# Performance work log

Measured on AMD Instinct MI355X. Metric: run time of the kernel, lower is better.

The kernel has to match this reference:

```python
import jax, jax.numpy as jnp
import numpy as np

ALPHA = 0.2  # LeakyReLU negative slope


def setup_inputs() -> dict:
    key = jax.random.key(0)
    ks = jax.random.split(key, 6)
    B, N, F_IN, F_OUT = 4, 4096, 128, 128
    return {
        "input": jax.random.normal(ks[0], (B, N, F_IN), dtype=jnp.float32),
        "adj": jax.random.uniform(ks[1], (B, N, N), dtype=jnp.float32),
        "W": jax.random.normal(ks[2], (F_IN, F_OUT), dtype=jnp.float32) * (np.sqrt(2.0) / np.sqrt(F_IN)),
        "a1": jax.random.normal(ks[3], (F_OUT, 1), dtype=jnp.float32) * 0.1,
        "a2": jax.random.normal(ks[4], (F_OUT, 1), dtype=jnp.float32) * 0.1,
        "bias": jax.random.normal(ks[5], (N, F_OUT), dtype=jnp.float32) * 0.02,
    }


def reference(input, adj, W, a1, a2, bias):
    # h = X @ W : [B, N, F_out]
    h = jnp.einsum("bnf,fo->bno", input, W)
    # additive attention scores: e[b,i,j] = leakyrelu(f1[b,i] + f2[b,j])
    f1 = h @ a1            # [B, N, 1]
    f2 = h @ a2            # [B, N, 1]
    e = f1 + jnp.swapaxes(f2, 1, 2)        # [B, N, N]
    e = jnp.where(e >= 0, e, ALPHA * e)    # LeakyReLU
    # NOTE: original multiplies adj into scores (not -inf masking) and
    # softmaxes over dim=1 (the first node axis), faithfully reproduced.
    attention = jax.nn.softmax(adj * e, axis=1)  # [B, N, N]
    # dropout p=0 / eval mode -> identity
    h_prime = jnp.einsum("bij,bjo->bio", attention, h) + bias[None, :, :]
    # in_features == out_features -> plain residual
    return h_prime + input
```

## Files before the change

kernel.cpp:

```cpp
#include <hip/hip_runtime.h>
#include <hip/hip_bf16.h>

typedef short short8 __attribute__((ext_vector_type(8)));
typedef float f32x4 __attribute__((ext_vector_type(4)));
typedef unsigned short u16;
typedef u16 u16x4 __attribute__((ext_vector_type(4)));
typedef u16 u16x8 __attribute__((ext_vector_type(8)));

static constexpr float kAlpha = 0.2f;

static __device__ inline u16 f2bf(float f) {
  __hip_bfloat16 h = __float2bfloat16(f);
  return *reinterpret_cast<u16*>(&h);
}
static __device__ inline float bf2f(u16 v) {
  unsigned int u = ((unsigned int)v) << 16;
  return __uint_as_float(u);
}

__global__ __launch_bounds__(256) void k1_hW(const float* __restrict__ X,
                                             const float* __restrict__ W,
                                             const float* __restrict__ a1,
                                             const float* __restrict__ a2,
                                             u16* __restrict__ hbT,
                                             float* __restrict__ f1,
                                             float* __restrict__ f2) {
  int row0 = blockIdx.x * 8;
  int o = threadIdx.x & 127;
  int g = threadIdx.x >> 7;
  __shared__ float Xs[8][128];
#pragma unroll
  for (int s = 0; s < 4; ++s) {
    int idx = threadIdx.x + s * 256;
    Xs[idx >> 7][idx & 127] = X[(size_t)row0 * 128 + idx];
  }
  __syncthreads();
  float acc[4] = {0.f, 0.f, 0.f, 0.f};
  for (int k = 0; k < 128; ++k) {
    float w = W[k * 128 + o];
#pragma unroll
    for (int s = 0; s < 4; ++s) acc[s] += Xs[g + 2 * s][k] * w;
  }
  int b = row0 >> 12;
  int n0 = row0 & 4095;
#pragma unroll
  for (int s = 0; s < 4; ++s)
    hbT[((size_t)b * 128 + o) * 4096 + n0 + g + 2 * s] = f2bf(acc[s]);

  float a1o = a1[o], a2o = a2[o];
  __syncthreads();
#pragma unroll
  for (int s = 0; s < 4; ++s) Xs[g + 2 * s][o] = acc[s] * a1o;
  __syncthreads();
  int r = threadIdx.x >> 5, c = threadIdx.x & 31;
  float s1 = Xs[r][c] + Xs[r][c + 32] + Xs[r][c + 64] + Xs[r][c + 96];
  s1 += __shfl_xor(s1, 1);
  s1 += __shfl_xor(s1, 2);
  s1 += __shfl_xor(s1, 4);
  s1 += __shfl_xor(s1, 8);
  s1 += __shfl_xor(s1, 16);
  if (c == 0) f1[b * 4096 + n0 + r] = s1;
  __syncthreads();
#pragma unroll
  for (int s = 0; s < 4; ++s) Xs[g + 2 * s][o] = acc[s] * a2o;
  __syncthreads();
  float s2 = Xs[r][c] + Xs[r][c + 32] + Xs[r][c + 64] + Xs[r][c + 96];
  s2 += __shfl_xor(s2, 1);
  s2 += __shfl_xor(s2, 2);
  s2 += __shfl_xor(s2, 4);
  s2 += __shfl_xor(s2, 8);
  s2 += __shfl_xor(s2, 16);
  if (c == 0) f2[b * 4096 + n0 + r] = s2;
}

__global__ __launch_bounds__(256) void k2_dpart(const float* __restrict__ adj,
                                                const float* __restrict__ f1,
                                                const float* __restrict__ f2,
                                                float* __restrict__ dpart) {
  int bid = blockIdx.x;
  int ic = bid & 31;
  int jt = (bid >> 5) & 15;
  int b = bid >> 9;
  int t = threadIdx.x;
  int c = t & 63, r = t >> 6;
  int j = jt * 256 + c * 4;
  const size_t badj = (size_t)b * 4096 * 4096;
  f32x4 f2v = *reinterpret_cast<const f32x4*>(&f2[b * 4096 + j]);
  const float* f1p = f1 + b * 4096;
  int row0 = ic * 128 + r;
  f32x4 sum = (f32x4){0.f, 0.f, 0.f, 0.f};
#pragma unroll 8
  for (int s = 0; s < 32; ++s) {
    int row = row0 + 4 * s;
    f32x4 a = *reinterpret_cast<const f32x4*>(&adj[badj + (size_t)row * 4096 + j]);
    float f1r = f1p[row];
#pragma unroll
    for (int k = 0; k < 4; ++k) {
      float e = f1r + f2v[k];
      e = e >= 0.f ? e : kAlpha * e;
      sum[k] += __expf(a[k] * e);
    }
  }
  __shared__ f32x4 red[256];
  red[t] = sum;
  __syncthreads();
  if (t < 64) {
    f32x4 tt = red[t] + red[t + 64] + red[t + 128] + red[t + 192];
    *reinterpret_cast<f32x4*>(&dpart[(size_t)(b * 32 + ic) * 4096 + j]) = tt;
  }
}

__global__ __launch_bounds__(256) void k2b_scale(const float* __restrict__ dpart,
                                                 const u16* __restrict__ hbT,
                                                 u16* __restrict__ hs) {
  int bid = blockIdx.x;
  int og = bid & 7;
  int jb = (bid >> 3) & 15;
  int b = bid >> 7;
  int j = jb * 256 + threadIdx.x;
  float s = 0.f;
#pragma unroll
  for (int ic = 0; ic < 32; ++ic) s += dpart[(size_t)(b * 32 + ic) * 4096 + j];
  float rd = 1.0f / s;
  const u16* src = hbT + (size_t)b * 128 * 4096 + j;
  u16* dst = hs + (size_t)b * 128 * 4096 + j;
#pragma unroll 4
  for (int o = og * 16; o < og * 16 + 16; ++o) {
    dst[(size_t)o * 4096] = f2bf(bf2f(src[(size_t)o * 4096]) * rd);
  }
}

#define LROWW 72
#define BARRIER()                                      \
  {                                                    \
    asm volatile("s_waitcnt lgkmcnt(0)" ::: "memory"); \
    __builtin_amdgcn_s_barrier();                      \
  }
__global__ __launch_bounds__(512) void k3w(const float* __restrict__ adj,
                                           const u16* __restrict__ hs,
                                           const float* __restrict__ f1,
                                           const float* __restrict__ f2,
                                           float* __restrict__ parts) {
  int bid0 = blockIdx.x;
  int bid = ((bid0 & 7) << 5) | (bid0 >> 3);
  int b = bid >> 6;
  int it = (bid >> 2) & 15;
  int jq = bid & 3;
  int i0 = it * 256;
  int jbase = jq * 1024;
  int t = threadIdx.x;
  int lane = t & 63;
  int w = t >> 6;
  int rw = w & 3;
  int cw = w >> 2;

  __shared__ u16 As[2][256 * LROWW];
  __shared__ u16 Bs[2][128 * LROWW];

  const size_t badj = (size_t)b * 4096 * 4096;
  const u16* hb = hs + (size_t)b * 128 * 4096;
  const float* f2b = f2 + b * 4096;

  int r0 = t >> 4;
  int c0 = (t & 15) * 4;
  int bo = t >> 2;
  int bc0 = (t & 3) * 16;

  float f1v[8];
#pragma unroll
  for (int u = 0; u < 8; ++u) f1v[u] = f1[b * 4096 + i0 + r0 + 32 * u];

  int l15 = lane & 15;
  int l8 = (lane >> 4) * 8;

  f32x4 acc[4][4];
#pragma unroll
  for (int rg = 0; rg < 4; ++rg)
#pragma unroll
    for (int n = 0; n < 4; ++n) acc[rg][n] = (f32x4){0.f, 0.f, 0.f, 0.f};

  const float* ap0 = adj + badj + (size_t)(i0 + r0) * 4096 + c0;

  f32x4 raA0, raA1, raA2, raA3, raA4, raA5, raA6, raA7;
  f32x4 raB0, raB1, raB2, raB3, raB4, raB5, raB6, raB7;
  f32x4 rfA, rfB;
  u16x8 rbA0, rbA1, rbB0, rbB1;

#define PF(S, JO)                                                         \
  {                                                                       \
    int jj = jbase + ((JO) & 1023);    \
    const float* ap = ap0 + jj;                                           \
    ra##S##0 = *reinterpret_cast<const f32x4*>(ap);                       \
    ra##S##1 = *reinterpret_cast<const f32x4*>(ap + (size_t)1 * 131072);  \
    ra##S##2 = *reinterpret_cast<const f32x4*>(ap + (size_t)2 * 131072);  \
    ra##S##3 = *reinterpret_cast<const f32x4*>(ap + (size_t)3 * 131072);  \
    ra##S##4 = *reinterpret_cast<const f32x4*>(ap + (size_t)4 * 131072);  \
    ra##S##5 = *reinterpret_cast<const f32x4*>(ap + (size_t)5 * 131072);  \
    ra##S##6 = *reinterpret_cast<const f32x4*>(ap + (size_t)6 * 131072);  \
    ra##S##7 = *reinterpret_cast<const f32x4*>(ap + (size_t)7 * 131072);  \
    rf##S = *reinterpret_cast<const f32x4*>(f2b + jj + c0);               \
    const u16* bp = hb + (size_t)bo * 4096 + jj + bc0;                    \
    rb##S##0 = *reinterpret_cast<const u16x8*>(bp);                       \
    rb##S##1 = *reinterpret_cast<const u16x8*>(bp + 8);                   \
  }

#define STU(S, U, BUF)                                                    \
  {                                                                       \
    u16x4 pv;                                                             \
    _Pragma("unroll") for (int k = 0; k < 4; ++k) {                       \
      float e = f1v[U] + rf##S[k];                                        \
      e = e >= 0.f ? e : kAlpha * e;                                      \
      pv[k] = f2bf(__expf(ra##S##U[k] * e));                              \
    }                                                                     \
    *reinterpret_cast<u16x4*>(&As[BUF][(r0 + 32 * U) * LROWW + c0]) = pv; \
  }

#define STORE(S, BUF)                                                     \
  {                                                                       \
    STU(S, 0, BUF) STU(S, 1, BUF) STU(S, 2, BUF) STU(S, 3, BUF)           \
    STU(S, 4, BUF) STU(S, 5, BUF) STU(S, 6, BUF) STU(S, 7, BUF)           \
    *reinterpret_cast<u16x8*>(&Bs[BUF][bo * LROWW + bc0]) = rb##S##0;     \
    *reinterpret_cast<u16x8*>(&Bs[BUF][bo * LROWW + bc0 + 8]) = rb##S##1; \
  }

#define DOMFMA(BUF)                                                                \
  {                                                                                \
    _Pragma("unroll") for (int kk = 0; kk < 64; kk += 32) {                        \
      short8 af0 = *reinterpret_cast<const short8*>(                               \
          &As[BUF][(rw * 64 + 0 * 16 + l15) * LROWW + kk + l8]);                   \
      short8 af1 = *reinterpret_cast<const short8*>(                               \
          &As[BUF][(rw * 64 + 1 * 16 + l15) * LROWW + kk + l8]);                   \
      short8 af2 = *reinterpret_cast<const short8*>(                               \
          &As[BUF][(rw * 64 + 2 * 16 + l15) * LROWW + kk + l8]);                   \
      short8 af3 = *reinterpret_cast<const short8*>(                               \
          &As[BUF][(rw * 64 + 3 * 16 + l15) * LROWW + kk + l8]);                   \
      _Pragma("unroll") for (int n = 0; n < 4; ++n) {                              \
        short8 bf = *reinterpret_cast<const short8*>(                              \
            &Bs[BUF][(cw * 64 + n * 16 + l15) * LROWW + kk + l8]);                 \
        acc[0][n] = __builtin_amdgcn_mfma_f32_16x16x32_bf16(af0, bf, acc[0][n], 0, 0, 0); \
        acc[1][n] = __builtin_amdgcn_mfma_f32_16x16x32_bf16(af1, bf, acc[1][n], 0, 0, 0); \
        acc[2][n] = __builtin_amdgcn_mfma_f32_16x16x32_bf16(af2, bf, acc[2][n], 0, 0, 0); \
        acc[3][n] = __builtin_amdgcn_mfma_f32_16x16x32_bf16(af3, bf, acc[3][n], 0, 0, 0); \
      }                                                                            \
    }                                                                              \
  }

  PF(A, 0);
  PF(B, 64);

  for (int j0 = 0; j0 < 1024; j0 += 128) {
    STORE(A, 0);
    BARRIER();
    DOMFMA(0);
    PF(A, j0 + 128);
    STORE(B, 1);
    BARRIER();
    DOMFMA(1);
    PF(B, j0 + 192);
  }

  float* pq = parts + (size_t)(b * 4 + jq) * 4096 * 128;
#pragma unroll
  for (int rg = 0; rg < 4; ++rg) {
#pragma unroll
    for (int n = 0; n < 4; ++n) {
      int o = cw * 64 + n * 16 + l15;
#pragma unroll
      for (int q = 0; q < 4; ++q) {
        int i = i0 + rw * 64 + rg * 16 + (lane >> 4) * 4 + q;
        pq[(size_t)i * 128 + o] = acc[rg][n][q];
      }
    }
  }
}

__global__ __launch_bounds__(256) void k4r(const float* __restrict__ parts,
                                           const float* __restrict__ bias,
                                           const float* __restrict__ input,
                                           float* __restrict__ out) {
  size_t v = (size_t)blockIdx.x * 256 + threadIdx.x;
  int b = (int)(v >> 17);
  size_t e = (v & 131071) * 4;
  const float* pb = parts + (size_t)b * 4 * 524288;
  f32x4 s = *reinterpret_cast<const f32x4*>(&pb[e]);
  s += *reinterpret_cast<const f32x4*>(&pb[e + 524288]);
  s += *reinterpret_cast<const f32x4*>(&pb[e + 2 * 524288]);
  s += *reinterpret_cast<const f32x4*>(&pb[e + 3 * 524288]);
  s += *reinterpret_cast<const f32x4*>(&bias[e]);
  size_t ge = (size_t)b * 524288 + e;
  s += *reinterpret_cast<const f32x4*>(&input[ge]);
  *reinterpret_cast<f32x4*>(&out[ge]) = s;
}

extern "C" void kernel_launch(void* const* d_in, const int* in_sizes, int n_in,
                              void* d_out, int out_size, void* d_ws, size_t ws_size,
                              hipStream_t stream) {
  const float* input = (const float*)d_in[0];
  const float* adj = (const float*)d_in[1];
  const float* W = (const float*)d_in[2];
  const float* a1 = (const float*)d_in[3];
  const float* a2 = (const float*)d_in[4];
  const float* bias = (const float*)d_in[5];
  float* out = (float*)d_out;

  char* ws = (char*)d_ws;
  u16* hbT = (u16*)(ws);
  float* f1 = (float*)(ws + 4194304);
  float* f2 = (float*)(ws + 4259840);
  float* dpart = (float*)(ws + 4325376);
  u16* hs = (u16*)(ws + 6422528);
  float* parts = (float*)(ws + 10616832);

  k1_hW<<<2048, 256, 0, stream>>>(input, W, a1, a2, hbT, f1, f2);
  k2_dpart<<<2048, 256, 0, stream>>>(adj, f1, f2, dpart);
  k2b_scale<<<512, 256, 0, stream>>>(dpart, hbT, hs);
  k3w<<<256, 512, 0, stream>>>(adj, hs, f1, f2, parts);
  k4r<<<2048, 256, 0, stream>>>(parts, bias, input, out);
}
```

Baseline: 136.9 us.

## Fold softmax column normalization into attention GEMM and store partials as bf16

Removes the separate k2b_scale kernel. The GEMM kernel now reduces the per-column denominators into shared memory and multiplies each exp value by its column's reciprocal before the bf16 conversion. The split-K partial outputs are also written as bf16 instead of fp32, which halves that intermediate traffic in k3w and k4r. This saves one launch and one pass over h, but adds per-block denominator reduction work and precision loss in the partial sums.

```diff
diff --git a/kernel.cpp b/kernel.cpp
--- a/kernel.cpp
+++ b/kernel.cpp
@@ -110,26 +110,6 @@
   }
 }
 
-__global__ __launch_bounds__(256) void k2b_scale(const float* __restrict__ dpart,
-                                                 const u16* __restrict__ hbT,
-                                                 u16* __restrict__ hs) {
-  int bid = blockIdx.x;
-  int og = bid & 7;
-  int jb = (bid >> 3) & 15;
-  int b = bid >> 7;
-  int j = jb * 256 + threadIdx.x;
-  float s = 0.f;
-#pragma unroll
-  for (int ic = 0; ic < 32; ++ic) s += dpart[(size_t)(b * 32 + ic) * 4096 + j];
-  float rd = 1.0f / s;
-  const u16* src = hbT + (size_t)b * 128 * 4096 + j;
-  u16* dst = hs + (size_t)b * 128 * 4096 + j;
-#pragma unroll 4
-  for (int o = og * 16; o < og * 16 + 16; ++o) {
-    dst[(size_t)o * 4096] = f2bf(bf2f(src[(size_t)o * 4096]) * rd);
-  }
-}
-
 #define LROWW 72
 #define BARRIER()                                      \
   {                                                    \
@@ -137,10 +117,11 @@
     __builtin_amdgcn_s_barrier();                      \
   }
 __global__ __launch_bounds__(512) void k3w(const float* __restrict__ adj,
-                                           const u16* __restrict__ hs,
+                                           const u16* __restrict__ hbT,
                                            const float* __restrict__ f1,
                                            const float* __restrict__ f2,
-                                           float* __restrict__ parts) {
+                                           const float* __restrict__ dpart,
+                                           u16* __restrict__ parts) {
   int bid0 = blockIdx.x;
   int bid = ((bid0 & 7) << 5) | (bid0 >> 3);
   int b = bid >> 6;
@@ -156,9 +137,10 @@
 
   __shared__ u16 As[2][256 * LROWW];
   __shared__ u16 Bs[2][128 * LROWW];
+  __shared__ float rds[1024];
 
   const size_t badj = (size_t)b * 4096 * 4096;
-  const u16* hb = hs + (size_t)b * 128 * 4096;
+  const u16* hb = hbT + (size_t)b * 128 * 4096;
   const float* f2b = f2 + b * 4096;
 
   int r0 = t >> 4;
@@ -210,13 +192,14 @@
     _Pragma("unroll") for (int k = 0; k < 4; ++k) {                       \
       float e = f1v[U] + rf##S[k];                                        \
       e = e >= 0.f ? e : kAlpha * e;                                      \
-      pv[k] = f2bf(__expf(ra##S##U[k] * e));                              \
+      pv[k] = f2bf(__expf(ra##S##U[k] * e) * rdv[k]);                     \
     }                                                                     \
     *reinterpret_cast<u16x4*>(&As[BUF][(r0 + 32 * U) * LROWW + c0]) = pv; \
   }
 
-#define STORE(S, BUF)                                                     \
+#define STORE(S, BUF, JO)                                                 \
   {                                                                       \
+    f32x4 rdv = *reinterpret_cast<const f32x4*>(&rds[((JO) & 1023) + c0]);\
     STU(S, 0, BUF) STU(S, 1, BUF) STU(S, 2, BUF) STU(S, 3, BUF)           \
     STU(S, 4, BUF) STU(S, 5, BUF) STU(S, 6, BUF) STU(S, 7, BUF)           \
     *reinterpret_cast<u16x8*>(&Bs[BUF][bo * LROWW + bc0]) = rb##S##0;     \
@@ -248,18 +231,31 @@
   PF(A, 0);
   PF(B, 64);
 
+  {
+    const float* dp = dpart + (size_t)b * 32 * 4096 + jbase;
+#pragma unroll
+    for (int u = 0; u < 2; ++u) {
+      int jj = t * 2 + u;
+      float s = 0.f;
+#pragma unroll
+      for (int ic = 0; ic < 32; ++ic) s += dp[(size_t)ic * 4096 + jj];
+      rds[jj] = 1.0f / s;
+    }
+  }
+  __syncthreads();
+
   for (int j0 = 0; j0 < 1024; j0 += 128) {
-    STORE(A, 0);
+    STORE(A, 0, j0);
     BARRIER();
     DOMFMA(0);
     PF(A, j0 + 128);
-    STORE(B, 1);
+    STORE(B, 1, j0 + 64);
     BARRIER();
     DOMFMA(1);
     PF(B, j0 + 192);
   }
 
-  float* pq = parts + (size_t)(b * 4 + jq) * 4096 * 128;
+  u16* pq = parts + (size_t)(b * 4 + jq) * 4096 * 128;
 #pragma unroll
   for (int rg = 0; rg < 4; ++rg) {
 #pragma unroll
@@ -268,27 +264,31 @@
 #pragma unroll
       for (int q = 0; q < 4; ++q) {
         int i = i0 + rw * 64 + rg * 16 + (lane >> 4) * 4 + q;
-        pq[(size_t)i * 128 + o] = acc[rg][n][q];
+        pq[(size_t)i * 128 + o] = f2bf(acc[rg][n][q]);
       }
     }
   }
 }
 
-__global__ __launch_bounds__(256) void k4r(const float* __restrict__ parts,
+__global__ __launch_bounds__(256) void k4r(const u16* __restrict__ parts,
                                            const float* __restrict__ bias,
                                            const float* __restrict__ input,
                                            float* __restrict__ out) {
   size_t v = (size_t)blockIdx.x * 256 + threadIdx.x;
   int b = (int)(v >> 17);
   size_t e = (v & 131071) * 4;
-  const float* pb = parts + (size_t)b * 4 * 524288;
-  f32x4 s = *reinterpret_cast<const f32x4*>(&pb[e]);
-  s += *reinterpret_cast<const f32x4*>(&pb[e + 524288]);
-  s += *reinterpret_cast<const f32x4*>(&pb[e + 2 * 524288]);
-  s += *reinterpret_cast<const f32x4*>(&pb[e + 3 * 524288]);
-  s += *reinterpret_cast<const f32x4*>(&bias[e]);
+  const u16* pb = parts + (size_t)b * 4 * 524288;
+  u16x4 p0 = *reinterpret_cast<const u16x4*>(&pb[e]);
+  u16x4 p1 = *reinterpret_cast<const u16x4*>(&pb[e + 524288]);
+  u16x4 p2 = *reinterpret_cast<const u16x4*>(&pb[e + 2 * 524288]);
+  u16x4 p3 = *reinterpret_cast<const u16x4*>(&pb[e + 3 * 524288]);
+  f32x4 bv = *reinterpret_cast<const f32x4*>(&bias[e]);
   size_t ge = (size_t)b * 524288 + e;
-  s += *reinterpret_cast<const f32x4*>(&input[ge]);
+  f32x4 iv = *reinterpret_cast<const f32x4*>(&input[ge]);
+  f32x4 s;
+#pragma unroll
+  for (int k = 0; k < 4; ++k)
+    s[k] = bf2f(p0[k]) + bf2f(p1[k]) + bf2f(p2[k]) + bf2f(p3[k]) + bv[k] + iv[k];
   *reinterpret_cast<f32x4*>(&out[ge]) = s;
 }
 
@@ -308,12 +308,10 @@
   float* f1 = (float*)(ws + 4194304);
   float* f2 = (float*)(ws + 4259840);
   float* dpart = (float*)(ws + 4325376);
-  u16* hs = (u16*)(ws + 6422528);
-  float* parts = (float*)(ws + 10616832);
+  u16* parts = (u16*)(ws + 6422528);
 
   k1_hW<<<2048, 256, 0, stream>>>(input, W, a1, a2, hbT, f1, f2);
   k2_dpart<<<2048, 256, 0, stream>>>(adj, f1, f2, dpart);
-  k2b_scale<<<512, 256, 0, stream>>>(dpart, hbT, hs);
-  k3w<<<256, 512, 0, stream>>>(adj, hs, f1, f2, parts);
+  k3w<<<256, 512, 0, stream>>>(adj, hbT, f1, f2, dpart, parts);
   k4r<<<2048, 256, 0, stream>>>(parts, bias, input, out);
 }
```

Result: no change. 134.2 us (-2.0%).
